# Kernel optimization log

Hardware: AMD Instinct MI355X
Metric: run time of the kernel (lower is better)

The kernel has to match this reference:

```python
import jax, jax.numpy as jnp
import numpy as np
from jax import lax

MAX_LEN = 40
SOS_ID = 2
VOCAB, EMB, HID, CTX = 32000, 512, 1024, 64
H2 = HID // 2
B, S = 256, 128


def gru_cell(x, h, wih, whh, bih, bhh):
    # PyTorch GRU equations: gates ordered (r, z, n)
    gx = x @ wih.T + bih
    gh = h @ whh.T + bhh
    rx, zx, nx = jnp.split(gx, 3, axis=-1)
    rh, zh, nh = jnp.split(gh, 3, axis=-1)
    r = jax.nn.sigmoid(rx + rh)
    z = jax.nn.sigmoid(zx + zh)
    n = jnp.tanh(nx + r * nh)
    return (1.0 - z) * n + z * h


def setup_inputs() -> dict:
    key = jax.random.key(0)
    ks = jax.random.split(key, 16)
    sd = 0.02
    emb_table = jax.random.normal(ks[0], (VOCAB, EMB), jnp.float32) * sd
    emb_table = emb_table.at[0].set(0.0)  # padding_idx=0
    def w(k, shape):
        return jax.random.normal(k, shape, jnp.float32) * sd
    inp = {
        "input_ids": jax.random.randint(ks[1], (B, S), 0, VOCAB),
        "context_vec": jax.random.normal(ks[2], (B, CTX), jnp.float32),
        "emb_table": emb_table,
        # encoder fwd direction
        "enc_wih_f": w(ks[3], (3 * H2, EMB)),
        "enc_whh_f": w(ks[4], (3 * H2, H2)),
        "enc_bih_f": w(ks[5], (3 * H2,)),
        "enc_bhh_f": w(ks[6], (3 * H2,)),
        # encoder bwd direction
        "enc_wih_b": w(ks[7], (3 * H2, EMB)),
        "enc_whh_b": w(ks[8], (3 * H2, H2)),
        "enc_bih_b": w(ks[9], (3 * H2,)),
        "enc_bhh_b": w(ks[10], (3 * H2,)),
        # decoder GRU: input = emb + hidden + context
        "dec_wih": w(ks[11], (3 * HID, EMB + HID + CTX)),
        "dec_whh": w(ks[12], (3 * HID, HID)),
        "dec_bih": w(ks[13], (3 * HID,)),
        "dec_bhh": w(ks[14], (3 * HID,)),
        "wout": w(ks[15], (VOCAB, HID)),
        "bout": jnp.zeros((VOCAB,), jnp.float32),
    }
    return inp


def reference(input_ids, context_vec, emb_table,
              enc_wih_f, enc_whh_f, enc_bih_f, enc_bhh_f,
              enc_wih_b, enc_whh_b, enc_bih_b, enc_bhh_b,
              dec_wih, dec_whh, dec_bih, dec_bhh, wout, bout):
    b = input_ids.shape[0]
    emb = emb_table[input_ids]                      # [B,S,E]
    emb_t = jnp.swapaxes(emb, 0, 1)                 # [S,B,E]

    def enc_f(h, x):
        return gru_cell(x, h, enc_wih_f, enc_whh_f, enc_bih_f, enc_bhh_f), None

    def enc_b(h, x):
        return gru_cell(x, h, enc_wih_b, enc_whh_b, enc_bih_b, enc_bhh_b), None

    h0 = jnp.zeros((b, H2), emb.dtype)
    hf, _ = lax.scan(enc_f, h0, emb_t)
    hb, _ = lax.scan(enc_b, h0, emb_t[::-1])
    # replicate torch's h_n.view(batch, -1) on a (2,B,H2) tensor (contiguous reshape)
    encoder_ctx = jnp.stack([hf, hb], axis=0).reshape(b, HID)   # [B,HID]

    ctx = jnp.concatenate([encoder_ctx, context_vec], axis=-1)  # [B,HID+CTX]
    h_dec0 = jnp.zeros((b, HID), emb.dtype)
    prev0 = jnp.full((b,), SOS_ID, dtype=jnp.int32)

    def dec_step(carry, _):
        h, prev = carry
        x = jnp.concatenate([emb_table[prev], ctx], axis=-1)
        h = gru_cell(x, h, dec_wih, dec_whh, dec_bih, dec_bhh)
        logits = h @ wout.T + bout                  # [B,V]
        probs = jax.nn.softmax(logits, axis=-1)
        nxt = jnp.argmax(probs, axis=-1).astype(jnp.int32)
        sel = jnp.take_along_axis(probs, nxt[:, None], axis=1)[:, 0]
        lp = jnp.log(sel + 1e-12)
        return (h, nxt), (nxt, lp)

    (_, _), (toks, lps) = lax.scan(dec_step, (h_dec0, prev0), None, length=MAX_LEN)
    return toks.T, lps.T   # [B,MAX_LEN] tokens, [B,MAX_LEN] log-probs
```

## Files before the change

kernel.cpp:

```cpp
#include <hip/hip_runtime.h>
#include <hip/hip_bf16.h>
#include <math.h>

#define B_    256
#define S_    128
#define EMB_  512
#define H2_   512
#define HID_  1024
#define CTX_  64
#define VOC_  32000
#define TMAX_ 40
#define SOS_  2

typedef unsigned short u16;
typedef __attribute__((ext_vector_type(8))) short short8;
typedef __attribute__((ext_vector_type(4))) float f32x4;

__device__ __forceinline__ float4 ld4(const float* p) {
    return *reinterpret_cast<const float4*>(p);
}
__device__ __forceinline__ float sigmoidf_(float x) { return 1.f / (1.f + expf(-x)); }
__device__ __forceinline__ u16 f2bf(float x) {
    union { float f; unsigned int u; } v; v.f = x;
    unsigned int r = v.u + 0x7FFFu + ((v.u >> 16) & 1u);
    return (u16)(r >> 16);
}
__device__ __forceinline__ unsigned pk2(float a, float b) {
    float2 t; t.x = a; t.y = b;
    __hip_bfloat162 h = __float22bfloat162_rn(t);
    return *reinterpret_cast<unsigned*>(&h);
}
__device__ __forceinline__ void merge_top2(float& v1, int& i1, float& v2, int& i2,
                                           float ov1, int oi1, float ov2, int oi2)
{
    if (ov1 > v1 || (ov1 == v1 && oi1 < i1)) {
        float tv = v1; int ti = i1;
        v1 = ov1; i1 = oi1;
        if (ov2 > tv || (ov2 == tv && oi2 < ti)) { v2 = ov2; i2 = oi2; }
        else                                     { v2 = tv;  i2 = ti;  }
    } else {
        if (ov1 > v2 || (ov1 == v2 && oi1 < i2)) { v2 = ov1; i2 = oi1; }
    }
}

template<int BM, int BN, int TM, int TN, int AMODE, int BGATHER, int BIASM>
__launch_bounds__(256)
__global__ void gemm_nt(const float* __restrict__ Ap,
                        const int*   __restrict__ ids,
                        const float* __restrict__ Ex,
                        const float* __restrict__ Bp, int ldb, int bofs,
                        const float* __restrict__ bias,
                        const float* __restrict__ addsrc,
                        float* __restrict__ Cp, int ldc,
                        int lda, int K, int s_base, int sdir)
{
    constexpr int BK = 32;
    __shared__ float As[BK][BM + 4];
    __shared__ float Bs[BK][BN + 4];
    const int t  = threadIdx.x;
    const int tx = t & 15, ty = t >> 4;
    const int m_base = blockIdx.y * BM;
    const int n_base = blockIdx.x * BN;

    float acc[TM][TN];
#pragma unroll
    for (int i = 0; i < TM; ++i)
#pragma unroll
        for (int j = 0; j < TN; ++j) acc[i][j] = 0.f;

    constexpr int A_PER = BM * BK / 4 / 256;
    constexpr int B_PER = BN * BK / 4 / 256;

    for (int k0 = 0; k0 < K; k0 += BK) {
#pragma unroll
        for (int j = 0; j < A_PER; ++j) {
            int f   = t + j * 256;
            int row = f >> 3;
            int kk  = (f & 7) << 2;
            int m   = m_base + row;
            float4 v;
            if constexpr (AMODE == 0) {
                v = ld4(Ap + (size_t)m * lda + k0 + kk);
            } else if constexpr (AMODE == 3) {
                int id = ids[m];
                v = ld4(Ex + (size_t)id * EMB_ + k0 + kk);
            } else {
                int k = k0 + kk;
                if (k < HID_) v = ld4(Ap + (size_t)m * HID_ + k);
                else          v = ld4(Ex + (size_t)m * CTX_ + (k - HID_));
            }
            As[kk + 0][row] = v.x; As[kk + 1][row] = v.y;
            As[kk + 2][row] = v.z; As[kk + 3][row] = v.w;
        }
#pragma unroll
        for (int j = 0; j < B_PER; ++j) {
            int f   = t + j * 256;
            int row = f >> 3;
            int kk  = (f & 7) << 2;
            float4 v;
            if constexpr (BGATHER == 1) {
                int n = n_base + row;
                int s = n >> 8, b = n & 255;
                int id = ids[b * S_ + s_base + sdir * s];
                v = ld4(Ex + (size_t)id * EMB_ + k0 + kk);
            } else {
                v = ld4(Bp + (size_t)(n_base + row) * ldb + bofs + k0 + kk);
            }
            Bs[kk + 0][row] = v.x; Bs[kk + 1][row] = v.y;
            Bs[kk + 2][row] = v.z; Bs[kk + 3][row] = v.w;
        }
        __syncthreads();
#pragma unroll
        for (int kk = 0; kk < BK; ++kk) {
            float a[TM], b[TN];
            *(float4*)&a[0] = ld4(&As[kk][ty * TM]);
            if constexpr (TM == 8) *(float4*)&a[4] = ld4(&As[kk][ty * TM + 4]);
            *(float4*)&b[0] = ld4(&Bs[kk][tx * TN]);
            if constexpr (TN == 8) *(float4*)&b[4] = ld4(&Bs[kk][tx * TN + 4]);
#pragma unroll
            for (int i = 0; i < TM; ++i)
#pragma unroll
                for (int j = 0; j < TN; ++j) acc[i][j] += a[i] * b[j];
        }
        __syncthreads();
    }
#pragma unroll
    for (int i = 0; i < TM; ++i) {
        int m = m_base + ty * TM + i;
#pragma unroll
        for (int j = 0; j < TN; ++j) {
            int n = n_base + tx * TN + j;
            float v = acc[i][j];
            if (bias) v += BIASM ? bias[m] : bias[n];
            if (addsrc) v += addsrc[(size_t)m * ldc + n];
            Cp[(size_t)m * ldc + n] = v;
        }
    }
}

__launch_bounds__(256)
__global__ void enc_gx2(const float* __restrict__ wih_f, const float* __restrict__ wih_b,
                        const float* __restrict__ bih_f, const float* __restrict__ bih_b,
                        const int* __restrict__ ids, const float* __restrict__ emb,
                        float* __restrict__ gx_f, float* __restrict__ gx_b, int c)
{
    constexpr int BK = 32;
    __shared__ float As[BK][132];
    __shared__ float Bs[BK][132];
    const int t  = threadIdx.x;
    const int tx = t & 15, ty = t >> 4;
    const int dz = blockIdx.z;
    const float* W    = dz ? wih_b : wih_f;
    const float* bias = dz ? bih_b : bih_f;
    float*       Cp   = dz ? gx_b : gx_f;
    const int s_base  = dz ? (127 - 16 * c) : (16 * c);
    const int sdir    = dz ? -1 : 1;
    const int m_base = blockIdx.y * 128;
    const int n_base = blockIdx.x * 128;

    float acc[8][8];
#pragma unroll
    for (int i = 0; i < 8; ++i)
#pragma unroll
        for (int j = 0; j < 8; ++j) acc[i][j] = 0.f;

    for (int k0 = 0; k0 < 512; k0 += BK) {
#pragma unroll
        for (int j = 0; j < 4; ++j) {
            int f   = t + j * 256;
            int row = f >> 3;
            int kk  = (f & 7) << 2;
            int m   = m_base + row;
            int s   = m >> 8, b = m & 255;
            int id  = ids[b * S_ + s_base + sdir * s];
            float4 v = ld4(emb + (size_t)id * EMB_ + k0 + kk);
            As[kk + 0][row] = v.x; As[kk + 1][row] = v.y;
            As[kk + 2][row] = v.z; As[kk + 3][row] = v.w;
        }
#pragma unroll
        for (int j = 0; j < 4; ++j) {
            int f   = t + j * 256;
            int row = f >> 3;
            int kk  = (f & 7) << 2;
            float4 v = ld4(W + (size_t)(n_base + row) * 512 + k0 + kk);
            Bs[kk + 0][row] = v.x; Bs[kk + 1][row] = v.y;
            Bs[kk + 2][row] = v.z; Bs[kk + 3][row] = v.w;
        }
        __syncthreads();
#pragma unroll
        for (int kk = 0; kk < BK; ++kk) {
            float a[8], b[8];
            *(float4*)&a[0] = ld4(&As[kk][ty * 8]);
            *(float4*)&a[4] = ld4(&As[kk][ty * 8 + 4]);
            *(float4*)&b[0] = ld4(&Bs[kk][tx * 8]);
            *(float4*)&b[4] = ld4(&Bs[kk][tx * 8 + 4]);
#pragma unroll
            for (int i = 0; i < 8; ++i)
#pragma unroll
                for (int j = 0; j < 8; ++j) acc[i][j] += a[i] * b[j];
        }
        __syncthreads();
    }
#pragma unroll
    for (int i = 0; i < 8; ++i) {
        int m = m_base + ty * 8 + i;
#pragma unroll
        for (int j = 0; j < 8; ++j) {
            int n = n_base + tx * 8 + j;
            Cp[(size_t)m * 1536 + n] = acc[i][j] + bias[n];
        }
    }
}

__global__ void whh_trans(const float* __restrict__ whh_f, const float* __restrict__ whh_b,
                          float* __restrict__ whhX_f, float* __restrict__ whhX_b)
{
    int idx = blockIdx.x * 256 + threadIdx.x;
    const float* src = blockIdx.y ? whh_b : whh_f;
    float*       dst = blockIdx.y ? whhX_b : whhX_f;
    int k  = idx / 1536;
    int cc = idx - k * 1536;
    int u  = cc / 3;
    int g  = cc - u * 3;
    dst[idx] = src[(size_t)(g * 512 + u) * 512 + k];
}

__launch_bounds__(512)
__global__ void enc_rec(const float* __restrict__ gxc_f, const float* __restrict__ gxc_b,
                        const float* __restrict__ whhX_f, const float* __restrict__ whhX_b,
                        const float* __restrict__ bhh_f, const float* __restrict__ bhh_b,
                        float* __restrict__ hT, int nsteps)
{
    __shared__ __align__(16) float hbuf[2][512][4];
    __shared__ float red[256][25];
    const int bid = blockIdx.x;
    const int xcd = bid & 7;
    const int dir = xcd >> 2;
    const int local = (bid >> 3) * 4 + (xcd & 3);
    const int r0 = local * 4;
    const float* gx  = dir ? gxc_b : gxc_f;
    const float* whx = dir ? whhX_b : whhX_f;
    const float* bhh = dir ? bhh_b : bhh_f;
    float* hTd = hT + (size_t)dir * (256 * 512);

    const int t  = threadIdx.x;
    const int kh = t >> 8;
    const int tu = t & 255;
    const int k_base = kh << 8;

    for (int i = t; i < 2048; i += 512) {
        int r = i >> 9, u = i & 511;
        hbuf[0][u][r] = hTd[(size_t)(r0 + r) * 512 + u];
    }
    float bh[2][3];
#pragma unroll
    for (int uu = 0; uu < 2; ++uu)
#pragma unroll
        for (int g = 0; g < 3; ++g)
            bh[uu][g] = bhh[g * 512 + tu * 2 + uu];
    __syncthreads();

    for (int st = 0; st < nsteps; ++st) {
        const int cur = st & 1, nxt = cur ^ 1;
        float acc[2][3][4];
#pragma unroll
        for (int uu = 0; uu < 2; ++uu)
#pragma unroll
            for (int g = 0; g < 3; ++g)
#pragma unroll
                for (int r = 0; r < 4; ++r) acc[uu][g][r] = 0.f;

        const float* wp = whx + (size_t)k_base * 1536 + tu * 6;
#pragma unroll 4
        for (int kk = 0; kk < 256; ++kk) {
            float4 hv = *(const float4*)&hbuf[cur][k_base + kk][0];
            float2 w0 = *(const float2*)(wp + 0);
            float2 w1 = *(const float2*)(wp + 2);
            float2 w2 = *(const float2*)(wp + 4);
            const float* hvp = (const float*)&hv;
#pragma unroll
            for (int r = 0; r < 4; ++r) {
                float h = hvp[r];
                acc[0][0][r] += w0.x * h;
                acc[0][1][r] += w0.y * h;
                acc[0][2][r] += w1.x * h;
                acc[1][0][r] += w1.y * h;
                acc[1][1][r] += w2.x * h;
                acc[1][2][r] += w2.y * h;
            }
            wp += 1536;
        }

        if (kh) {
#pragma unroll
            for (int uu = 0; uu < 2; ++uu)
#pragma unroll
                for (int g = 0; g < 3; ++g)
#pragma unroll
                    for (int r = 0; r < 4; ++r)
                        red[tu][(uu * 3 + g) * 4 + r] = acc[uu][g][r];
        }
        __syncthreads();
        if (!kh) {
#pragma unroll
            for (int uu = 0; uu < 2; ++uu)
#pragma unroll
                for (int g = 0; g < 3; ++g)
#pragma unroll
                    for (int r = 0; r < 4; ++r)
                        acc[uu][g][r] += red[tu][(uu * 3 + g) * 4 + r];
            float2 gxv[3][4];
#pragma unroll
            for (int g = 0; g < 3; ++g)
#pragma unroll
                for (int r = 0; r < 4; ++r)
                    gxv[g][r] = *(const float2*)&gx[(size_t)((st << 8) + r0 + r) * 1536
                                                    + (g << 9) + (tu << 1)];
#pragma unroll
            for (int uu = 0; uu < 2; ++uu) {
                int u = tu * 2 + uu;
#pragma unroll
                for (int r = 0; r < 4; ++r) {
                    float gr = uu ? gxv[0][r].y : gxv[0][r].x;
                    float gz = uu ? gxv[1][r].y : gxv[1][r].x;
                    float gn = uu ? gxv[2][r].y : gxv[2][r].x;
                    float hold = hbuf[cur][u][r];
                    float rg = sigmoidf_(gr + acc[uu][0][r] + bh[uu][0]);
                    float zg = sigmoidf_(gz + acc[uu][1][r] + bh[uu][1]);
                    float ng = tanhf(gn + rg * (acc[uu][2][r] + bh[uu][2]));
                    hbuf[nxt][u][r] = (1.f - zg) * ng + zg * hold;
                }
            }
        }
        __syncthreads();
    }

    const int lb = nsteps & 1;
    for (int i = t; i < 2048; i += 512) {
        int r = i >> 9, u = i & 511;
        hTd[(size_t)(r0 + r) * 512 + u] = hbuf[lb][u][r];
    }
}

__global__ void zerof(float* __restrict__ p, int n)
{
    int i = blockIdx.x * 256 + threadIdx.x;
    if (i < n) p[i] = 0.f;
}

__global__ void init_dec(float* __restrict__ hdec, u16* __restrict__ hbf, int* __restrict__ prev)
{
    int i = blockIdx.x * 256 + threadIdx.x;
    hdec[i] = 0.f; hbf[i] = 0;
    if (i < B_) prev[i] = SOS_;
}

__global__ void hcat_build(const float* __restrict__ hT, float* __restrict__ hcat)
{
    int idx = blockIdx.x * 256 + threadIdx.x;
    int b = idx >> 10, k = idx & 1023;
    int d = b >> 7;
    int rr = ((2 * b) & 255) + (k >> 9);
    int kk = k & 511;
    hcat[idx] = hT[(size_t)d * 131072 + (size_t)rr * 512 + kk];
}

__launch_bounds__(256)
__global__ void dec_gemm2(const float* __restrict__ hdec, const int* __restrict__ prev,
                          const float* __restrict__ emb,
                          const float* __restrict__ dwhh, const float* __restrict__ dwih,
                          const float* __restrict__ dbhh, const float* __restrict__ gctx,
                          float* __restrict__ ghbuf, float* __restrict__ gibuf)
{
    constexpr int BK = 32;
    __shared__ float As[BK][68];
    __shared__ float Bs[BK][68];
    const int t  = threadIdx.x;
    const int tx = t & 15, ty = t >> 4;
    const bool isH = blockIdx.y < 4;
    const int m_base = (isH ? blockIdx.y : (blockIdx.y - 4)) * 64;
    const int n_base = blockIdx.x * 64;
    const int K   = isH ? 1024 : 512;
    const float* Bp = isH ? dwhh : dwih;
    const int ldb  = isH ? 1024 : 1600;
    float* Cp = isH ? ghbuf : gibuf;

    float acc[4][4];
#pragma unroll
    for (int i = 0; i < 4; ++i)
#pragma unroll
        for (int j = 0; j < 4; ++j) acc[i][j] = 0.f;

    for (int k0 = 0; k0 < K; k0 += BK) {
#pragma unroll
        for (int j = 0; j < 2; ++j) {
            int f   = t + j * 256;
            int row = f >> 3;
            int kk  = (f & 7) << 2;
            int m   = m_base + row;
            float4 v;
            if (isH) v = ld4(hdec + (size_t)m * HID_ + k0 + kk);
            else     v = ld4(emb + (size_t)prev[m] * EMB_ + k0 + kk);
            As[kk + 0][row] = v.x; As[kk + 1][row] = v.y;
            As[kk + 2][row] = v.z; As[kk + 3][row] = v.w;
            float4 w = ld4(Bp + (size_t)(n_base + row) * ldb + k0 + kk);
            Bs[kk + 0][row] = w.x; Bs[kk + 1][row] = w.y;
            Bs[kk + 2][row] = w.z; Bs[kk + 3][row] = w.w;
        }
        __syncthreads();
#pragma unroll
        for (int kk = 0; kk < BK; ++kk) {
            float a[4], b[4];
            *(float4*)&a[0] = ld4(&As[kk][ty * 4]);
            *(float4*)&b[0] = ld4(&Bs[kk][tx * 4]);
#pragma unroll
            for (int i = 0; i < 4; ++i)
#pragma unroll
                for (int j = 0; j < 4; ++j) acc[i][j] += a[i] * b[j];
        }
        __syncthreads();
    }
#pragma unroll
    for (int i = 0; i < 4; ++i) {
        int m = m_base + ty * 4 + i;
#pragma unroll
        for (int j = 0; j < 4; ++j) {
            int n = n_base + tx * 4 + j;
            float v = acc[i][j];
            if (isH) v += dbhh[n];
            else     v += gctx[(size_t)m * 3072 + n];
            Cp[(size_t)m * 3072 + n] = v;
        }
    }
}

__global__ void dec_combine(const float* __restrict__ gi, const float* __restrict__ gh,
                            float* __restrict__ hdec, u16* __restrict__ hbf)
{
    int idx = blockIdx.x * 256 + threadIdx.x;
    int b = idx >> 10, u = idx & 1023;
    size_t gb = (size_t)b * 3072;
    float r = sigmoidf_(gi[gb + u]            + gh[gb + u]);
    float z = sigmoidf_(gi[gb + HID_ + u]     + gh[gb + HID_ + u]);
    float n = tanhf    (gi[gb + 2 * HID_ + u] + r * gh[gb + 2 * HID_ + u]);
    float v = (1.f - z) * n + z * hdec[idx];
    hdec[idx] = v;
    hbf[idx] = f2bf(v);
}

__launch_bounds__(512)
__global__ void gemm_logits(const u16* __restrict__ A, const float* __restrict__ Wf,
                            const float* __restrict__ bias,
                            float* __restrict__ pmax, float* __restrict__ psum,
                            float* __restrict__ ptv, int* __restrict__ pti)
{
    __shared__ u16 As[256][72];
    __shared__ u16 Bs[128][72];
    const int t = threadIdx.x;
    const int lane = t & 63, wave = t >> 6;
    const int wm = (wave & 3) * 64, wn = (wave >> 2) * 64;
    const int n0 = blockIdx.x * 128;
    f32x4 acc[4][4];
#pragma unroll
    for (int i = 0; i < 4; ++i)
#pragma unroll
        for (int j = 0; j < 4; ++j) acc[i][j] = (f32x4){0.f, 0.f, 0.f, 0.f};
    const int arow = t >> 1, aoff = (t & 1) * 32;
    const int brow = t >> 2, boff = (t & 3) * 16;

    for (int k0 = 0; k0 < 1024; k0 += 64) {
#pragma unroll
        for (int q = 0; q < 4; ++q) {
            *(uint4*)&As[arow][aoff + q * 8] =
                *(const uint4*)(A + (size_t)arow * 1024 + k0 + aoff + q * 8);
        }
        const float* wr = Wf + (size_t)(n0 + brow) * 1024 + k0 + boff;
#pragma unroll
        for (int q = 0; q < 2; ++q) {
            float4 x = ld4(wr + q * 8);
            float4 y = ld4(wr + q * 8 + 4);
            uint4 o;
            o.x = pk2(x.x, x.y); o.y = pk2(x.z, x.w);
            o.z = pk2(y.x, y.y); o.w = pk2(y.z, y.w);
            *(uint4*)&Bs[brow][boff + q * 8] = o;
        }
        __syncthreads();
#pragma unroll
        for (int s = 0; s < 2; ++s) {
            short8 a[4], b[4];
            int j0 = s * 32 + (lane >> 4) * 8;
#pragma unroll
            for (int i = 0; i < 4; ++i) {
                a[i] = *(const short8*)&As[wm + i * 16 + (lane & 15)][j0];
                b[i] = *(const short8*)&Bs[wn + i * 16 + (lane & 15)][j0];
            }
#pragma unroll
            for (int i = 0; i < 4; ++i)
#pragma unroll
                for (int j = 0; j < 4; ++j)
                    acc[i][j] = __builtin_amdgcn_mfma_f32_16x16x32_bf16(a[i], b[j], acc[i][j], 0, 0, 0);
        }
        __syncthreads();
    }

    const int htile = blockIdx.x * 2 + (wn >> 6);
    float bn[4]; int jx[4];
#pragma unroll
    for (int j = 0; j < 4; ++j) { jx[j] = n0 + wn + j * 16 + (lane & 15); bn[j] = bias[jx[j]]; }
#pragma unroll
    for (int i = 0; i < 4; ++i) {
#pragma unroll
        for (int rr = 0; rr < 4; ++rr) {
            float v[4];
#pragma unroll
            for (int j = 0; j < 4; ++j) v[j] = acc[i][j][rr] + bn[j];
            float v1 = v[0], v2 = -3.4e38f; int i1 = jx[0], i2 = 0x7fffffff;
#pragma unroll
            for (int j = 1; j < 4; ++j) {
                if (v[j] > v1)      { v2 = v1; i2 = i1; v1 = v[j]; i1 = jx[j]; }
                else if (v[j] > v2) { v2 = v[j]; i2 = jx[j]; }
            }
#pragma unroll
            for (int mask = 1; mask <= 8; mask <<= 1) {
                float ov1 = __shfl_xor(v1, mask), ov2 = __shfl_xor(v2, mask);
                int   oi1 = __shfl_xor(i1, mask), oi2 = __shfl_xor(i2, mask);
                merge_top2(v1, i1, v2, i2, ov1, oi1, ov2, oi2);
            }
            float rmax = v1;
            float s = 0.f;
#pragma unroll
            for (int j = 0; j < 4; ++j) s += expf(v[j] - rmax);
#pragma unroll
            for (int mask = 1; mask <= 8; mask <<= 1) s += __shfl_xor(s, mask);
            if ((lane & 15) == 0) {
                int row = wm + i * 16 + (lane >> 4) * 4 + rr;
                size_t base = (size_t)row * 500 + htile;
                pmax[base] = rmax; psum[base] = s;
                ptv[base * 2] = v1; ptv[base * 2 + 1] = v2;
                pti[base * 2] = i1; pti[base * 2 + 1] = i2;
            }
        }
    }
}

__launch_bounds__(256)
__global__ void dec_reduce(const float* __restrict__ pmax, const float* __restrict__ psum,
                           const float* __restrict__ ptv, const int* __restrict__ pti,
                           const float* __restrict__ hdec, const float* __restrict__ wout,
                           const float* __restrict__ bout,
                           float* __restrict__ out, int* __restrict__ prev, int tstep)
{
    __shared__ float sv[256]; __shared__ int sti[256]; __shared__ int ssl[256];
    __shared__ float cvv[1000]; __shared__ int cii[1000];
    __shared__ float c8v[8]; __shared__ int c8i[8]; __shared__ float c8e[8];
    const int b = blockIdx.x, tid = threadIdx.x;
    const float* pm = pmax + (size_t)b * 500;
    const float* ps = psum + (size_t)b * 500;

    float m = -3.4e38f;
    for (int i = tid; i < 500; i += 256) m = fmaxf(m, pm[i]);
    sv[tid] = m; __syncthreads();
    for (int off = 128; off; off >>= 1) { if (tid < off) sv[tid] = fmaxf(sv[tid], sv[tid + off]); __syncthreads(); }
    float gmax = sv[0]; __syncthreads();

    float s = 0.f;
    for (int i = tid; i < 500; i += 256) s += ps[i] * expf(pm[i] - gmax);
    sv[tid] = s; __syncthreads();
    for (int off = 128; off; off >>= 1) { if (tid < off) sv[tid] += sv[tid + off]; __syncthreads(); }
    float gsum = sv[0]; __syncthreads();

    for (int i = tid; i < 1000; i += 256) { cvv[i] = ptv[(size_t)b * 1000 + i]; cii[i] = pti[(size_t)b * 1000 + i]; }
    __syncthreads();

    for (int c = 0; c < 8; ++c) {
        float bv = -3.4e38f; int bi = 0x7fffffff, bs = 0;
        for (int i = tid; i < 1000; i += 256) {
            float v = cvv[i]; int ix = cii[i];
            if (v > bv || (v == bv && ix < bi)) { bv = v; bi = ix; bs = i; }
        }
        sv[tid] = bv; sti[tid] = bi; ssl[tid] = bs; __syncthreads();
        for (int off = 128; off; off >>= 1) {
            if (tid < off) {
                if (sv[tid + off] > sv[tid] ||
                    (sv[tid + off] == sv[tid] && sti[tid + off] < sti[tid])) {
                    sv[tid] = sv[tid + off]; sti[tid] = sti[tid + off]; ssl[tid] = ssl[tid + off];
                }
            }
            __syncthreads();
        }
        if (tid == 0) { c8v[c] = sv[0]; c8i[c] = sti[0]; cvv[ssl[0]] = -3.4e38f; }
        __syncthreads();
    }

    {
        int lane = tid & 63, wv = tid >> 6;
        const float* hr = hdec + (size_t)b * HID_;
        for (int c = wv; c < 8; c += 4) {
            const float* wr = wout + (size_t)c8i[c] * HID_;
            float a = 0.f;
            for (int k = lane * 4; k < HID_; k += 256) {
                float4 x = ld4(hr + k), y = ld4(wr + k);
                a += x.x * y.x + x.y * y.y + x.z * y.z + x.w * y.w;
            }
#pragma unroll
            for (int off = 32; off; off >>= 1) a += __shfl_down(a, off);
            if (lane == 0) c8e[c] = a + bout[c8i[c]];
        }
    }
    __syncthreads();

    if (tid == 0) {
        float bv = c8e[0]; int bi = c8i[0]; float av = c8v[0];
        for (int c = 1; c < 8; ++c)
            if (c8e[c] > bv || (c8e[c] == bv && c8i[c] < bi)) { bv = c8e[c]; bi = c8i[c]; av = c8v[c]; }
        float p = expf(av - gmax) / gsum;
        float lp = logf(p + 1e-12f);
        out[(size_t)b * TMAX_ + tstep] = (float)bi;
        out[B_ * TMAX_ + (size_t)b * TMAX_ + tstep] = lp;
        prev[b] = bi;
    }
}

extern "C" void kernel_launch(void* const* d_in, const int* in_sizes, int n_in,
                              void* d_out, int out_size, void* d_ws, size_t ws_size,
                              hipStream_t stream)
{
    const int*   ids   = (const int*)  d_in[0];
    const float* cvec  = (const float*)d_in[1];
    const float* emb   = (const float*)d_in[2];
    const float* wih_f = (const float*)d_in[3];
    const float* whh_f = (const float*)d_in[4];
    const float* bih_f = (const float*)d_in[5];
    const float* bhh_f = (const float*)d_in[6];
    const float* wih_b = (const float*)d_in[7];
    const float* whh_b = (const float*)d_in[8];
    const float* bih_b = (const float*)d_in[9];
    const float* bhh_b = (const float*)d_in[10];
    const float* dwih  = (const float*)d_in[11];
    const float* dwhh  = (const float*)d_in[12];
    const float* dbih  = (const float*)d_in[13];
    const float* dbhh  = (const float*)d_in[14];
    const float* wout  = (const float*)d_in[15];
    const float* bout  = (const float*)d_in[16];
    float* out = (float*)d_out;

    float* w      = (float*)d_ws;
    float* gxc_f  = w;
    float* gxc_b  = w + 6291456;
    float* hT     = w + 12582912;
    float* hcat   = w + 12845056;
    float* hdec   = w + 13107200;
    float* gctx   = w + 13369344;
    u16*   hdecb  = (u16*)(w + 14155776);
    int*   prev   = (int*)(w + 14286848);
    float* whhX_f = w + 14287104;
    float* whhX_b = w + 15073536;
    float* gibuf  = gxc_f;
    float* ghbuf  = gxc_f + 786432;
    float* pmax   = gxc_f + 1572864;
    float* psum   = gxc_f + 1700864;
    float* ptv    = gxc_f + 1828864;
    int*   pti    = (int*)(gxc_f + 2084864);

    zerof<<<1024, 256, 0, stream>>>(hT, 262144);
    init_dec<<<1024, 256, 0, stream>>>(hdec, hdecb, prev);
    whh_trans<<<dim3(3072, 2), 256, 0, stream>>>(whh_f, whh_b, whhX_f, whhX_b);

    for (int c = 0; c < 8; ++c) {
        enc_gx2<<<dim3(12, 32, 2), 256, 0, stream>>>(
            wih_f, wih_b, bih_f, bih_b, ids, emb, gxc_f, gxc_b, c);
        enc_rec<<<128, 512, 0, stream>>>(
            gxc_f, gxc_b, whhX_f, whhX_b, bhh_f, bhh_b, hT, 16);
    }

    hcat_build<<<1024, 256, 0, stream>>>(hT, hcat);

    gemm_nt<64, 64, 4, 4, 2, 0, 0><<<dim3(48, 4), 256, 0, stream>>>(
        hcat, nullptr, cvec, dwih, 1600, 512, dbih, nullptr,
        gctx, 3072, 1024, 1088, 0, 0);

    for (int t = 0; t < TMAX_; ++t) {
        dec_gemm2<<<dim3(48, 8), 256, 0, stream>>>(
            hdec, prev, emb, dwhh, dwih, dbhh, gctx, ghbuf, gibuf);
        dec_combine<<<1024, 256, 0, stream>>>(gibuf, ghbuf, hdec, hdecb);
        gemm_logits<<<dim3(250, 1), 512, 0, stream>>>(hdecb, wout, bout,
                                                      pmax, psum, ptv, pti);
        dec_reduce<<<256, 256, 0, stream>>>(pmax, psum, ptv, pti,
                                            hdec, wout, bout, out, prev, t);
    }
}
```

Measured before the change: 11.46 ms.

## Fuse encoder input-projection GEMM with recurrence in one launch, software-pipelined by chunk

```diff
diff --git a/kernel.cpp b/kernel.cpp
--- a/kernel.cpp
+++ b/kernel.cpp
@@ -138,80 +138,6 @@
     }
 }
 
-__launch_bounds__(256)
-__global__ void enc_gx2(const float* __restrict__ wih_f, const float* __restrict__ wih_b,
-                        const float* __restrict__ bih_f, const float* __restrict__ bih_b,
-                        const int* __restrict__ ids, const float* __restrict__ emb,
-                        float* __restrict__ gx_f, float* __restrict__ gx_b, int c)
-{
-    constexpr int BK = 32;
-    __shared__ float As[BK][132];
-    __shared__ float Bs[BK][132];
-    const int t  = threadIdx.x;
-    const int tx = t & 15, ty = t >> 4;
-    const int dz = blockIdx.z;
-    const float* W    = dz ? wih_b : wih_f;
-    const float* bias = dz ? bih_b : bih_f;
-    float*       Cp   = dz ? gx_b : gx_f;
-    const int s_base  = dz ? (127 - 16 * c) : (16 * c);
-    const int sdir    = dz ? -1 : 1;
-    const int m_base = blockIdx.y * 128;
-    const int n_base = blockIdx.x * 128;
-
-    float acc[8][8];
-#pragma unroll
-    for (int i = 0; i < 8; ++i)
-#pragma unroll
-        for (int j = 0; j < 8; ++j) acc[i][j] = 0.f;
-
-    for (int k0 = 0; k0 < 512; k0 += BK) {
-#pragma unroll
-        for (int j = 0; j < 4; ++j) {
-            int f   = t + j * 256;
-            int row = f >> 3;
-            int kk  = (f & 7) << 2;
-            int m   = m_base + row;
-            int s   = m >> 8, b = m & 255;
-            int id  = ids[b * S_ + s_base + sdir * s];
-            float4 v = ld4(emb + (size_t)id * EMB_ + k0 + kk);
-            As[kk + 0][row] = v.x; As[kk + 1][row] = v.y;
-            As[kk + 2][row] = v.z; As[kk + 3][row] = v.w;
-        }
-#pragma unroll
-        for (int j = 0; j < 4; ++j) {
-            int f   = t + j * 256;
-            int row = f >> 3;
-            int kk  = (f & 7) << 2;
-            float4 v = ld4(W + (size_t)(n_base + row) * 512 + k0 + kk);
-            Bs[kk + 0][row] = v.x; Bs[kk + 1][row] = v.y;
-            Bs[kk + 2][row] = v.z; Bs[kk + 3][row] = v.w;
-        }
-        __syncthreads();
-#pragma unroll
-        for (int kk = 0; kk < BK; ++kk) {
-            float a[8], b[8];
-            *(float4*)&a[0] = ld4(&As[kk][ty * 8]);
-            *(float4*)&a[4] = ld4(&As[kk][ty * 8 + 4]);
-            *(float4*)&b[0] = ld4(&Bs[kk][tx * 8]);
-            *(float4*)&b[4] = ld4(&Bs[kk][tx * 8 + 4]);
-#pragma unroll
-            for (int i = 0; i < 8; ++i)
-#pragma unroll
-                for (int j = 0; j < 8; ++j) acc[i][j] += a[i] * b[j];
-        }
-        __syncthreads();
-    }
-#pragma unroll
-    for (int i = 0; i < 8; ++i) {
-        int m = m_base + ty * 8 + i;
-#pragma unroll
-        for (int j = 0; j < 8; ++j) {
-            int n = n_base + tx * 8 + j;
-            Cp[(size_t)m * 1536 + n] = acc[i][j] + bias[n];
-        }
-    }
-}
-
 __global__ void whh_trans(const float* __restrict__ whh_f, const float* __restrict__ whh_b,
                           float* __restrict__ whhX_f, float* __restrict__ whhX_b)
 {
@@ -225,32 +151,106 @@
     dst[idx] = src[(size_t)(g * 512 + u) * 512 + k];
 }
 
+#define RECBLK 128
+
+union EncSM {
+    struct { float hbuf[2][512][4]; float red[256][25]; } rec;
+    struct { float As[32][132]; float Bs[32][132]; } gx;
+};
+
 __launch_bounds__(512)
-__global__ void enc_rec(const float* __restrict__ gxc_f, const float* __restrict__ gxc_b,
-                        const float* __restrict__ whhX_f, const float* __restrict__ whhX_b,
-                        const float* __restrict__ bhh_f, const float* __restrict__ bhh_b,
-                        float* __restrict__ hT, int nsteps)
-{
-    __shared__ __align__(16) float hbuf[2][512][4];
-    __shared__ float red[256][25];
+__global__ void enc_fused(const float* __restrict__ grec_f, const float* __restrict__ grec_b,
+                          float* __restrict__ gout_f, float* __restrict__ gout_b,
+                          const float* __restrict__ whhX_f, const float* __restrict__ whhX_b,
+                          const float* __restrict__ bhh_f, const float* __restrict__ bhh_b,
+                          const float* __restrict__ wih_f, const float* __restrict__ wih_b,
+                          const float* __restrict__ bih_f, const float* __restrict__ bih_b,
+                          const int* __restrict__ ids, const float* __restrict__ emb,
+                          float* __restrict__ hT, int do_rec, int gx_chunk, int nsteps)
+{
+    __shared__ __align__(16) EncSM sm;
+    const int t = threadIdx.x;
+
+    if (blockIdx.x >= RECBLK) {
+        if (gx_chunk < 0) return;
+        const int tt  = blockIdx.x - RECBLK;
+        const int dz  = tt >= 192;
+        const int t192 = dz ? tt - 192 : tt;
+        const int m_base = (t192 & 15) * 128;
+        const int n_base = (t192 >> 4) * 128;
+        const float* W    = dz ? wih_b : wih_f;
+        const float* bias = dz ? bih_b : bih_f;
+        float*       Cp   = dz ? gout_b : gout_f;
+        const int s_base  = dz ? (127 - 8 * gx_chunk) : (8 * gx_chunk);
+        const int sdir    = dz ? -1 : 1;
+        const int tx = t & 31, ty = t >> 5;
+
+        float acc[8][4];
+#pragma unroll
+        for (int i = 0; i < 8; ++i)
+#pragma unroll
+            for (int j = 0; j < 4; ++j) acc[i][j] = 0.f;
+
+        for (int k0 = 0; k0 < 512; k0 += 32) {
+#pragma unroll
+            for (int j = 0; j < 2; ++j) {
+                int f   = t + j * 512;
+                int row = f >> 3;
+                int kk  = (f & 7) << 2;
+                int m   = m_base + row;
+                int s   = m >> 8, b = m & 255;
+                int id  = ids[b * S_ + s_base + sdir * s];
+                float4 v = ld4(emb + (size_t)id * EMB_ + k0 + kk);
+                sm.gx.As[kk + 0][row] = v.x; sm.gx.As[kk + 1][row] = v.y;
+                sm.gx.As[kk + 2][row] = v.z; sm.gx.As[kk + 3][row] = v.w;
+                float4 wv = ld4(W + (size_t)(n_base + row) * 512 + k0 + kk);
+                sm.gx.Bs[kk + 0][row] = wv.x; sm.gx.Bs[kk + 1][row] = wv.y;
+                sm.gx.Bs[kk + 2][row] = wv.z; sm.gx.Bs[kk + 3][row] = wv.w;
+            }
+            __syncthreads();
+#pragma unroll
+            for (int kk = 0; kk < 32; ++kk) {
+                float a[8], b[4];
+                *(float4*)&a[0] = ld4(&sm.gx.As[kk][ty * 8]);
+                *(float4*)&a[4] = ld4(&sm.gx.As[kk][ty * 8 + 4]);
+                *(float4*)&b[0] = ld4(&sm.gx.Bs[kk][tx * 4]);
+#pragma unroll
+                for (int i = 0; i < 8; ++i)
+#pragma unroll
+                    for (int j = 0; j < 4; ++j) acc[i][j] += a[i] * b[j];
+            }
+            __syncthreads();
+        }
+#pragma unroll
+        for (int i = 0; i < 8; ++i) {
+            int m = m_base + ty * 8 + i;
+#pragma unroll
+            for (int j = 0; j < 4; ++j) {
+                int n = n_base + tx * 4 + j;
+                Cp[(size_t)m * 1536 + n] = acc[i][j] + bias[n];
+            }
+        }
+        return;
+    }
+
+    if (!do_rec) return;
     const int bid = blockIdx.x;
     const int xcd = bid & 7;
     const int dir = xcd >> 2;
     const int local = (bid >> 3) * 4 + (xcd & 3);
     const int r0 = local * 4;
-    const float* gx  = dir ? gxc_b : gxc_f;
+    const float* gx  = dir ? grec_b : grec_f;
     const float* whx = dir ? whhX_b : whhX_f;
     const float* bhh = dir ? bhh_b : bhh_f;
     float* hTd = hT + (size_t)dir * (256 * 512);
 
-    const int t  = threadIdx.x;
     const int kh = t >> 8;
     const int tu = t & 255;
     const int k_base = kh << 8;
 
     for (int i = t; i < 2048; i += 512) {
         int r = i >> 9, u = i & 511;
-        hbuf[0][u][r] = hTd[(size_t)(r0 + r) * 512 + u];
+        sm.rec.hbuf[0][u][r] = hTd[(size_t)(r0 + r) * 512 + u];
     }
     float bh[2][3];
 #pragma unroll
@@ -262,6 +262,17 @@
 
     for (int st = 0; st < nsteps; ++st) {
         const int cur = st & 1, nxt = cur ^ 1;
+
+        float2 gxv[3][4];
+        if (!kh) {
+#pragma unroll
+            for (int g = 0; g < 3; ++g)
+#pragma unroll
+                for (int r = 0; r < 4; ++r)
+                    gxv[g][r] = *(const float2*)&gx[(size_t)((st << 8) + r0 + r) * 1536
+                                                    + (g << 9) + (tu << 1)];
+        }
+
         float acc[2][3][4];
 #pragma unroll
         for (int uu = 0; uu < 2; ++uu)
@@ -273,7 +284,7 @@
         const float* wp = whx + (size_t)k_base * 1536 + tu * 6;
 #pragma unroll 4
         for (int kk = 0; kk < 256; ++kk) {
-            float4 hv = *(const float4*)&hbuf[cur][k_base + kk][0];
+            float4 hv = *(const float4*)&sm.rec.hbuf[cur][k_base + kk][0];
             float2 w0 = *(const float2*)(wp + 0);
             float2 w1 = *(const float2*)(wp + 2);
             float2 w2 = *(const float2*)(wp + 4);
@@ -298,7 +309,7 @@
                 for (int g = 0; g < 3; ++g)
 #pragma unroll
                     for (int r = 0; r < 4; ++r)
-                        red[tu][(uu * 3 + g) * 4 + r] = acc[uu][g][r];
+                        sm.rec.red[tu][(uu * 3 + g) * 4 + r] = acc[uu][g][r];
         }
         __syncthreads();
         if (!kh) {
@@ -308,14 +319,7 @@
                 for (int g = 0; g < 3; ++g)
 #pragma unroll
                     for (int r = 0; r < 4; ++r)
-                        acc[uu][g][r] += red[tu][(uu * 3 + g) * 4 + r];
-            float2 gxv[3][4];
-#pragma unroll
-            for (int g = 0; g < 3; ++g)
-#pragma unroll
-                for (int r = 0; r < 4; ++r)
-                    gxv[g][r] = *(const float2*)&gx[(size_t)((st << 8) + r0 + r) * 1536
-                                                    + (g << 9) + (tu << 1)];
+                        acc[uu][g][r] += sm.rec.red[tu][(uu * 3 + g) * 4 + r];
 #pragma unroll
             for (int uu = 0; uu < 2; ++uu) {
                 int u = tu * 2 + uu;
@@ -324,11 +328,11 @@
                     float gr = uu ? gxv[0][r].y : gxv[0][r].x;
                     float gz = uu ? gxv[1][r].y : gxv[1][r].x;
                     float gn = uu ? gxv[2][r].y : gxv[2][r].x;
-                    float hold = hbuf[cur][u][r];
+                    float hold = sm.rec.hbuf[cur][u][r];
                     float rg = sigmoidf_(gr + acc[uu][0][r] + bh[uu][0]);
                     float zg = sigmoidf_(gz + acc[uu][1][r] + bh[uu][1]);
                     float ng = tanhf(gn + rg * (acc[uu][2][r] + bh[uu][2]));
-                    hbuf[nxt][u][r] = (1.f - zg) * ng + zg * hold;
+                    sm.rec.hbuf[nxt][u][r] = (1.f - zg) * ng + zg * hold;
                 }
             }
         }
@@ -338,7 +342,7 @@
     const int lb = nsteps & 1;
     for (int i = t; i < 2048; i += 512) {
         int r = i >> 9, u = i & 511;
-        hTd[(size_t)(r0 + r) * 512 + u] = hbuf[lb][u][r];
+        hTd[(size_t)(r0 + r) * 512 + u] = sm.rec.hbuf[lb][u][r];
     }
 }
 
@@ -645,8 +649,10 @@
     float* out = (float*)d_out;
 
     float* w      = (float*)d_ws;
-    float* gxc_f  = w;
-    float* gxc_b  = w + 6291456;
+    float* buf0_f = w;
+    float* buf0_b = w + 3145728;
+    float* buf1_f = w + 6291456;
+    float* buf1_b = w + 9437184;
     float* hT     = w + 12582912;
     float* hcat   = w + 12845056;
     float* hdec   = w + 13107200;
@@ -655,23 +661,32 @@
     int*   prev   = (int*)(w + 14286848);
     float* whhX_f = w + 14287104;
     float* whhX_b = w + 15073536;
-    float* gibuf  = gxc_f;
-    float* ghbuf  = gxc_f + 786432;
-    float* pmax   = gxc_f + 1572864;
-    float* psum   = gxc_f + 1700864;
-    float* ptv    = gxc_f + 1828864;
-    int*   pti    = (int*)(gxc_f + 2084864);
+    float* gibuf  = buf0_f;
+    float* ghbuf  = buf0_f + 786432;
+    float* pmax   = buf0_f + 1572864;
+    float* psum   = buf0_f + 1700864;
+    float* ptv    = buf0_f + 1828864;
+    int*   pti    = (int*)(buf0_f + 2084864);
 
     zerof<<<1024, 256, 0, stream>>>(hT, 262144);
     init_dec<<<1024, 256, 0, stream>>>(hdec, hdecb, prev);
     whh_trans<<<dim3(3072, 2), 256, 0, stream>>>(whh_f, whh_b, whhX_f, whhX_b);
 
-    for (int c = 0; c < 8; ++c) {
-        enc_gx2<<<dim3(12, 32, 2), 256, 0, stream>>>(
-            wih_f, wih_b, bih_f, bih_b, ids, emb, gxc_f, gxc_b, c);
-        enc_rec<<<128, 512, 0, stream>>>(
-            gxc_f, gxc_b, whhX_f, whhX_b, bhh_f, bhh_b, hT, 16);
-    }
+    enc_fused<<<512, 512, 0, stream>>>(
+        buf0_f, buf0_b, buf0_f, buf0_b, whhX_f, whhX_b, bhh_f, bhh_b,
+        wih_f, wih_b, bih_f, bih_b, ids, emb, hT, 0, 0, 8);
+    for (int c = 1; c < 16; ++c) {
+        float* rf = ((c - 1) & 1) ? buf1_f : buf0_f;
+        float* rb = ((c - 1) & 1) ? buf1_b : buf0_b;
+        float* of = (c & 1) ? buf1_f : buf0_f;
+        float* ob = (c & 1) ? buf1_b : buf0_b;
+        enc_fused<<<512, 512, 0, stream>>>(
+            rf, rb, of, ob, whhX_f, whhX_b, bhh_f, bhh_b,
+            wih_f, wih_b, bih_f, bih_b, ids, emb, hT, 1, c, 8);
+    }
+    enc_fused<<<512, 512, 0, stream>>>(
+        buf1_f, buf1_b, buf1_f, buf1_b, whhX_f, whhX_b, bhh_f, bhh_b,
+        wih_f, wih_b, bih_f, bih_b, ids, emb, hT, 1, -1, 8);
 
     hcat_build<<<1024, 256, 0, stream>>>(hT, hcat);
 
```

Measured after the change: 10.65 ms. -7.1%, faster.
